# Optimization experiments

Measured on AMD Instinct MI355X. Metric: run time of the kernel, lower is better.

The kernel has to match this reference:

```python
import jax, jax.numpy as jnp
import numpy as np

B, S, E, H = 1, 2048, 1024, 16
D = E // H          # head_dim = 64
SM_SCALE = 0.5      # module default, not 1/sqrt(D)


def setup_inputs() -> dict:
    key = jax.random.key(0)
    ks = jax.random.split(key, 9)
    std = 0.02
    return {
        "x":  jax.random.normal(ks[0], (B, S, E), dtype=jnp.float32),
        "Wq": jax.random.normal(ks[1], (E, E), dtype=jnp.float32) * std,
        "bq": jnp.zeros((E,), dtype=jnp.float32),
        "Wk": jax.random.normal(ks[2], (E, E), dtype=jnp.float32) * std,
        "bk": jnp.zeros((E,), dtype=jnp.float32),
        "Wv": jax.random.normal(ks[3], (E, E), dtype=jnp.float32) * std,
        "bv": jnp.zeros((E,), dtype=jnp.float32),
        "Wo": jax.random.normal(ks[4], (E, E), dtype=jnp.float32) * std,
        "bo": jnp.zeros((E,), dtype=jnp.float32),
    }


def _split_heads(t):
    # [B,S,E] -> [B,H,S,D]
    b, s, _ = t.shape
    return jnp.transpose(t.reshape(b, s, H, D), (0, 2, 1, 3))


def reference(x, Wq, bq, Wk, bk, Wv, bv, Wo, bo):
    # Projections in fp32, then cast to bf16 (matches module's .astype(bf16))
    q = _split_heads((x @ Wq + bq).astype(jnp.bfloat16))
    k = _split_heads((x @ Wk + bk).astype(jnp.bfloat16))
    v = _split_heads((x @ Wv + bv).astype(jnp.bfloat16))

    # Blockwise loop in the original is mathematically full causal attention
    scores = jnp.einsum("bhqd,bhkd->bhqk", q, k) * SM_SCALE  # [B,H,S,S] bf16
    causal = jnp.tril(jnp.ones((S, S), dtype=bool))
    scores = jnp.where(causal[None, None, :, :], scores, -jnp.inf)
    probs = jax.nn.softmax(scores, axis=-1)
    out = jnp.einsum("bhqk,bhkd->bhqd", probs, v)            # [B,H,S,D]

    out = jnp.transpose(out, (0, 2, 1, 3)).reshape(B, S, E)
    # dropout off (is_training=False / rate=0); final projection in fp32
    return out.astype(jnp.float32) @ Wo + bo
```

## Files before the change

kernel.cpp:

```cpp
#include <hip/hip_runtime.h>
#include <hip/hip_bf16.h>

#define S_LEN 2048
#define E_DIM 1024
#define NH    16
#define HD    64
#define SM_SCALE 0.5f

typedef short bf16x8_t __attribute__((ext_vector_type(8)));
typedef float f32x4_t  __attribute__((ext_vector_type(4)));
typedef __bf16 bf16x4_t __attribute__((ext_vector_type(4)));

static __device__ __forceinline__ unsigned short f2bf_bits(float f) {
    return __builtin_bit_cast(unsigned short, (__bf16)f);
}

#define GLD16(gp, lp) __builtin_amdgcn_global_load_lds(                       \
    (const __attribute__((address_space(1))) void*)(gp),                      \
    (__attribute__((address_space(3))) void*)(lp), 16, 0, 0)

__global__ void k_prep(const float* __restrict__ x,
                       const float* __restrict__ Wq, const float* __restrict__ Wk,
                       const float* __restrict__ Wv, const float* __restrict__ Wo,
                       __bf16* __restrict__ xb, __bf16* __restrict__ wt) {
    const int z = blockIdx.z;
    if (z < 4) {
        __shared__ float tile[32][33];
        const float* W = z == 0 ? Wq : z == 1 ? Wk : z == 2 ? Wv : Wo;
        __bf16* o = wt + (size_t)z * E_DIM * E_DIM;
        const int tx = threadIdx.x, ty = threadIdx.y;
        const int bx = blockIdx.x * 32, by = blockIdx.y * 32;
#pragma unroll
        for (int j = 0; j < 32; j += 8)
            tile[ty + j][tx] = W[(size_t)(by + ty + j) * E_DIM + bx + tx];
        __syncthreads();
#pragma unroll
        for (int j = 0; j < 32; j += 8)
            o[(size_t)(bx + ty + j) * E_DIM + by + tx] = (__bf16)tile[tx][ty + j];
    } else {
        const int bid = (z - 4) * 1024 + blockIdx.y * 32 + blockIdx.x;
        const int tid = threadIdx.y * 32 + threadIdx.x;
        const int i = bid * 256 + tid;
        const float4 v = ((const float4*)x)[i];
        bf16x4_t o4;
        o4.x = (__bf16)v.x; o4.y = (__bf16)v.y; o4.z = (__bf16)v.z; o4.w = (__bf16)v.w;
        ((bf16x4_t*)xb)[i] = o4;
    }
}

__global__ __launch_bounds__(256) void k_gemm_qkv(
    const __bf16* __restrict__ xb, const __bf16* __restrict__ wt,
    const float* __restrict__ bq, const float* __restrict__ bk, const float* __restrict__ bv,
    __bf16* __restrict__ qkv) {
    __shared__ __align__(16) unsigned short As[64 * 32];
    __shared__ __align__(16) unsigned short Bs[128 * 32];

    const int z = blockIdx.z;
    const __bf16* Bt = wt + (size_t)z * E_DIM * E_DIM;
    const float* bias = z == 0 ? bq : z == 1 ? bk : bv;
    __bf16* out = qkv + (size_t)z * NH * S_LEN * HD;

    const int tid = threadIdx.x, w = tid >> 6, l = tid & 63;
    const int lm = l & 15, q4 = l >> 4;
    const int bm = blockIdx.y, bn = blockIdx.x;
    const int wm = w >> 1, wn = w & 1;

    const int sm = (w << 4) + (l >> 2);
    const int skk = (l & 3) << 3;
    const __bf16* Ag = xb + (size_t)(bm * 64 + sm) * E_DIM + skk;
    const __bf16* Bg = Bt + (size_t)(bn * 128 + sm) * E_DIM + skk;
    unsigned short* AsW = As + (w << 9);
    unsigned short* BsW = Bs + (w << 9);

    f32x4_t acc[2][4];
#pragma unroll
    for (int i = 0; i < 2; i++)
#pragma unroll
        for (int j = 0; j < 4; j++) { acc[i][j].x = 0.f; acc[i][j].y = 0.f; acc[i][j].z = 0.f; acc[i][j].w = 0.f; }

    for (int k0 = 0; k0 < E_DIM; k0 += 32) {
        __syncthreads();
        GLD16(Ag + k0, AsW);
        GLD16(Bg + k0, BsW);
        GLD16(Bg + (size_t)64 * E_DIM + k0, BsW + 2048);
        __syncthreads();

        bf16x8_t af[2], bfr[4];
#pragma unroll
        for (int mt = 0; mt < 2; mt++)
            af[mt] = *(const bf16x8_t*)&As[(wm * 32 + mt * 16 + lm) * 32 + q4 * 8];
#pragma unroll
        for (int nt = 0; nt < 4; nt++)
            bfr[nt] = *(const bf16x8_t*)&Bs[(wn * 64 + nt * 16 + lm) * 32 + q4 * 8];
#pragma unroll
        for (int mt = 0; mt < 2; mt++)
#pragma unroll
            for (int nt = 0; nt < 4; nt++)
                acc[mt][nt] = __builtin_amdgcn_mfma_f32_16x16x32_bf16(af[mt], bfr[nt], acc[mt][nt], 0, 0, 0);
    }

#pragma unroll
    for (int nt = 0; nt < 4; nt++) {
        const int n = bn * 128 + wn * 64 + nt * 16 + lm;
        const float bval = bias[n];
        const int h = n >> 6, d = n & 63;
        if (z == 2) {
            const int t4 = d >> 4, flm = d & 15;
#pragma unroll
            for (int mt = 0; mt < 2; mt++) {
                const int q4p = (mt * 2 + (q4 >> 1)) & 3;
                const int j0 = (q4 & 1) * 4;
                __bf16* ob = out + ((((size_t)h * 32 + bm) * 4 + t4) * 2 + wm) * 512
                                 + (q4p * 16 + flm) * 8 + j0;
                union { unsigned short s[4]; uint2 u; } pk;
#pragma unroll
                for (int i = 0; i < 4; i++) pk.s[i] = f2bf_bits(acc[mt][nt][i] + bval);
                *(uint2*)ob = pk.u;
            }
        } else {
            const float scale = (z == 0) ? SM_SCALE : 1.0f;
            const int c = d >> 5, q4p = (d >> 3) & 3, j = d & 7;
#pragma unroll
            for (int mt = 0; mt < 2; mt++) {
                const int s0 = bm * 64 + wm * 32 + mt * 16;
                const int kt6 = s0 >> 6, t4 = (s0 >> 4) & 3;
                __bf16* ob = out + ((((size_t)h * 32 + kt6) * 4 + t4) * 2 + c) * 512
                                 + (q4p * 16 + q4 * 4) * 8 + j;
#pragma unroll
                for (int i = 0; i < 4; i++)
                    ob[i * 8] = (__bf16)((acc[mt][nt][i] + bval) * scale);
            }
        }
    }
}

__global__ __launch_bounds__(256, 2) void k_attn(
    const __bf16* __restrict__ Qf, const __bf16* __restrict__ Kf, const __bf16* __restrict__ Vf,
    __bf16* __restrict__ attn) {
    __shared__ __align__(16) unsigned short KVs[2][2][4096];
    __shared__ __align__(16) unsigned short Pl[4][16 * 72];

    const int b = blockIdx.x;
    int qt, h;
    if (b < 256) { qt = 16 + (b >> 4); h = b & 15; }
    else         { qt = 15 - ((b - 256) >> 4); h = (b - 256) & 15; }

    const int tid = threadIdx.x, w = tid >> 6, l = tid & 63;
    const int lm = l & 15, q4 = l >> 4;

    const __bf16* Qb = Qf + ((size_t)h * 32 + qt) * 4096;
    const __bf16* Kb = Kf + (size_t)h * 32 * 4096;
    const __bf16* Vb = Vf + (size_t)h * 32 * 4096;

    bf16x8_t qf[2];
#pragma unroll
    for (int c = 0; c < 2; c++)
        qf[c] = *(const bf16x8_t*)(Qb + ((w * 2 + c) << 9) + l * 8);

    float lacc = 0.f;
    f32x4_t oacc[4];
#pragma unroll
    for (int t = 0; t < 4; t++) { oacc[t].x = 0.f; oacc[t].y = 0.f; oacc[t].z = 0.f; oacc[t].w = 0.f; }

    unsigned short* Pw = Pl[w];

    {
        const __bf16* Kg = Kb;
        const __bf16* Vg = Vb;
        GLD16(Kg + (w << 9) + l * 8,      &KVs[0][0][(w << 9) + l * 8]);
        GLD16(Kg + ((w + 4) << 9) + l * 8, &KVs[0][0][((w + 4) << 9) + l * 8]);
        GLD16(Vg + (w << 9) + l * 8,      &KVs[0][1][(w << 9) + l * 8]);
        GLD16(Vg + ((w + 4) << 9) + l * 8, &KVs[0][1][((w + 4) << 9) + l * 8]);
    }
    __syncthreads();

    for (int s = 0; s <= qt; s++) {
        const int bb = s & 1;
        if (s < qt) {
            const __bf16* Kg = Kb + (size_t)(s + 1) * 4096;
            const __bf16* Vg = Vb + (size_t)(s + 1) * 4096;
            GLD16(Kg + (w << 9) + l * 8,      &KVs[bb ^ 1][0][(w << 9) + l * 8]);
            GLD16(Kg + ((w + 4) << 9) + l * 8, &KVs[bb ^ 1][0][((w + 4) << 9) + l * 8]);
            GLD16(Vg + (w << 9) + l * 8,      &KVs[bb ^ 1][1][(w << 9) + l * 8]);
            GLD16(Vg + ((w + 4) << 9) + l * 8, &KVs[bb ^ 1][1][((w + 4) << 9) + l * 8]);
        }

        f32x4_t st[4];
#pragma unroll
        for (int t = 0; t < 4; t++) { st[t].x = 0.f; st[t].y = 0.f; st[t].z = 0.f; st[t].w = 0.f; }
#pragma unroll
        for (int t = 0; t < 4; t++) {
            bf16x8_t kf0 = *(const bf16x8_t*)&KVs[bb][0][((t * 2 + 0) << 9) + l * 8];
            bf16x8_t kf1 = *(const bf16x8_t*)&KVs[bb][0][((t * 2 + 1) << 9) + l * 8];
            st[t] = __builtin_amdgcn_mfma_f32_16x16x32_bf16(kf0, qf[0], st[t], 0, 0, 0);
            st[t] = __builtin_amdgcn_mfma_f32_16x16x32_bf16(kf1, qf[1], st[t], 0, 0, 0);
        }
        if (s == qt) {
            const int rowl = w * 16 + lm;
#pragma unroll
            for (int t = 0; t < 4; t++)
#pragma unroll
                for (int i = 0; i < 4; i++) {
                    const int keyl = t * 16 + q4 * 4 + i;
                    st[t][i] = (keyl > rowl) ? 0.f : __expf(st[t][i]);
                }
        } else {
#pragma unroll
            for (int t = 0; t < 4; t++)
#pragma unroll
                for (int i = 0; i < 4; i++) st[t][i] = __expf(st[t][i]);
        }
#pragma unroll
        for (int t = 0; t < 4; t++)
            lacc += (st[t][0] + st[t][1]) + (st[t][2] + st[t][3]);
#pragma unroll
        for (int t = 0; t < 4; t++) {
            union { unsigned short s4[4]; uint2 u; } pk;
#pragma unroll
            for (int i = 0; i < 4; i++) pk.s4[i] = f2bf_bits(st[t][i]);
            *(uint2*)&Pw[lm * 72 + t * 16 + q4 * 4] = pk.u;
        }
#pragma unroll
        for (int c = 0; c < 2; c++) {
            bf16x8_t pf = *(const bf16x8_t*)&Pw[lm * 72 + c * 32 + q4 * 8];
#pragma unroll
            for (int t = 0; t < 4; t++) {
                bf16x8_t vf = *(const bf16x8_t*)&KVs[bb][1][((t * 2 + c) << 9) + l * 8];
                oacc[t] = __builtin_amdgcn_mfma_f32_16x16x32_bf16(vf, pf, oacc[t], 0, 0, 0);
            }
        }
        __syncthreads();
    }

    lacc += __shfl_xor(lacc, 16, 64);
    lacc += __shfl_xor(lacc, 32, 64);
    const float rl = 1.f / lacc;
    const int row = qt * 64 + w * 16 + lm;
#pragma unroll
    for (int t = 0; t < 4; t++) {
        union { unsigned short s4[4]; uint2 u; } pk;
#pragma unroll
        for (int i = 0; i < 4; i++) pk.s4[i] = f2bf_bits(oacc[t][i] * rl);
        *(uint2*)(attn + (size_t)row * E_DIM + h * HD + t * 16 + q4 * 4) = pk.u;
    }
}

__global__ __launch_bounds__(256) void k_gemm_out(
    const __bf16* __restrict__ A, const __bf16* __restrict__ Bt,
    const float* __restrict__ bias, float* __restrict__ out) {
    __shared__ __align__(16) unsigned short As[64 * 32];
    __shared__ __align__(16) unsigned short Bs[128 * 32];

    const int tid = threadIdx.x, w = tid >> 6, l = tid & 63;
    const int lm = l & 15, q4 = l >> 4;
    const int bm = blockIdx.y, bn = blockIdx.x;
    const int wm = w >> 1, wn = w & 1;

    const int sm = (w << 4) + (l >> 2);
    const int skk = (l & 3) << 3;
    const __bf16* Ag = A + (size_t)(bm * 64 + sm) * E_DIM + skk;
    const __bf16* Bg = Bt + (size_t)(bn * 128 + sm) * E_DIM + skk;
    unsigned short* AsW = As + (w << 9);
    unsigned short* BsW = Bs + (w << 9);

    f32x4_t acc[2][4];
#pragma unroll
    for (int i = 0; i < 2; i++)
#pragma unroll
        for (int j = 0; j < 4; j++) { acc[i][j].x = 0.f; acc[i][j].y = 0.f; acc[i][j].z = 0.f; acc[i][j].w = 0.f; }

    for (int k0 = 0; k0 < E_DIM; k0 += 32) {
        __syncthreads();
        GLD16(Ag + k0, AsW);
        GLD16(Bg + k0, BsW);
        GLD16(Bg + (size_t)64 * E_DIM + k0, BsW + 2048);
        __syncthreads();

        bf16x8_t af[2], bfr[4];
#pragma unroll
        for (int mt = 0; mt < 2; mt++)
            af[mt] = *(const bf16x8_t*)&As[(wm * 32 + mt * 16 + lm) * 32 + q4 * 8];
#pragma unroll
        for (int nt = 0; nt < 4; nt++)
            bfr[nt] = *(const bf16x8_t*)&Bs[(wn * 64 + nt * 16 + lm) * 32 + q4 * 8];
#pragma unroll
        for (int mt = 0; mt < 2; mt++)
#pragma unroll
            for (int nt = 0; nt < 4; nt++)
                acc[mt][nt] = __builtin_amdgcn_mfma_f32_16x16x32_bf16(af[mt], bfr[nt], acc[mt][nt], 0, 0, 0);
    }

#pragma unroll
    for (int nt = 0; nt < 4; nt++) {
        const int n = bn * 128 + wn * 64 + nt * 16 + lm;
        const float bval = bias[n];
#pragma unroll
        for (int mt = 0; mt < 2; mt++) {
            const int r0 = bm * 64 + wm * 32 + mt * 16 + q4 * 4;
#pragma unroll
            for (int i = 0; i < 4; i++)
                out[(size_t)(r0 + i) * E_DIM + n] = acc[mt][nt][i] + bval;
        }
    }
}

extern "C" void kernel_launch(void* const* d_in, const int* in_sizes, int n_in,
                              void* d_out, int out_size, void* d_ws, size_t ws_size,
                              hipStream_t stream) {
    const float* x  = (const float*)d_in[0];
    const float* Wq = (const float*)d_in[1];
    const float* bq = (const float*)d_in[2];
    const float* Wk = (const float*)d_in[3];
    const float* bk = (const float*)d_in[4];
    const float* Wv = (const float*)d_in[5];
    const float* bv = (const float*)d_in[6];
    const float* Wo = (const float*)d_in[7];
    const float* bo = (const float*)d_in[8];
    float* out = (float*)d_out;

    char* ws = (char*)d_ws;
    __bf16* xb   = (__bf16*)(ws);
    __bf16* wt   = (__bf16*)(ws + ((size_t)4  << 20));
    __bf16* qkv  = (__bf16*)(ws + ((size_t)12 << 20));
    __bf16* attn = (__bf16*)(ws + ((size_t)24 << 20));

    k_prep<<<dim3(32, 32, 6), dim3(32, 8), 0, stream>>>(x, Wq, Wk, Wv, Wo, xb, wt);
    k_gemm_qkv<<<dim3(E_DIM / 128, S_LEN / 64, 3), 256, 0, stream>>>(xb, wt, bq, bk, bv, qkv);
    k_attn<<<dim3(512), 256, 0, stream>>>(
        qkv, qkv + (size_t)NH * S_LEN * HD, qkv + (size_t)2 * NH * S_LEN * HD, attn);
    k_gemm_out<<<dim3(E_DIM / 128, S_LEN / 64), 256, 0, stream>>>(
        attn, wt + (size_t)3 * E_DIM * E_DIM, bo, out);
}
```

Measured before the change: 155.8 us.

## Enlarge QKV GEMM tile to 128x128 and double-buffer output projection GEMM

The QKV projection GEMM now computes 128x128 tiles per block, so each wave handles a 64x64 sub-tile with 16 MFMAs per k-step. This improves operand reuse from LDS and halves the grid, and the epilogue's head-tiled output index math is rewritten to match. The output projection GEMM gets double-buffered LDS with the next k-slice prefetched during MFMA work, which removes one barrier per iteration. The trade-offs are higher register and LDS use, and fewer blocks for the QKV GEMM (384), which may lower occupancy.

```diff
diff --git a/kernel.cpp b/kernel.cpp
--- a/kernel.cpp
+++ b/kernel.cpp
@@ -52,7 +52,7 @@
     const __bf16* __restrict__ xb, const __bf16* __restrict__ wt,
     const float* __restrict__ bq, const float* __restrict__ bk, const float* __restrict__ bv,
     __bf16* __restrict__ qkv) {
-    __shared__ __align__(16) unsigned short As[64 * 32];
+    __shared__ __align__(16) unsigned short As[128 * 32];
     __shared__ __align__(16) unsigned short Bs[128 * 32];
 
     const int z = blockIdx.z;
@@ -67,33 +67,34 @@
 
     const int sm = (w << 4) + (l >> 2);
     const int skk = (l & 3) << 3;
-    const __bf16* Ag = xb + (size_t)(bm * 64 + sm) * E_DIM + skk;
+    const __bf16* Ag = xb + (size_t)(bm * 128 + sm) * E_DIM + skk;
     const __bf16* Bg = Bt + (size_t)(bn * 128 + sm) * E_DIM + skk;
     unsigned short* AsW = As + (w << 9);
     unsigned short* BsW = Bs + (w << 9);
 
-    f32x4_t acc[2][4];
-#pragma unroll
-    for (int i = 0; i < 2; i++)
+    f32x4_t acc[4][4];
+#pragma unroll
+    for (int i = 0; i < 4; i++)
 #pragma unroll
         for (int j = 0; j < 4; j++) { acc[i][j].x = 0.f; acc[i][j].y = 0.f; acc[i][j].z = 0.f; acc[i][j].w = 0.f; }
 
     for (int k0 = 0; k0 < E_DIM; k0 += 32) {
         __syncthreads();
         GLD16(Ag + k0, AsW);
+        GLD16(Ag + (size_t)64 * E_DIM + k0, AsW + 2048);
         GLD16(Bg + k0, BsW);
         GLD16(Bg + (size_t)64 * E_DIM + k0, BsW + 2048);
         __syncthreads();
 
-        bf16x8_t af[2], bfr[4];
-#pragma unroll
-        for (int mt = 0; mt < 2; mt++)
-            af[mt] = *(const bf16x8_t*)&As[(wm * 32 + mt * 16 + lm) * 32 + q4 * 8];
+        bf16x8_t af[4], bfr[4];
+#pragma unroll
+        for (int mt = 0; mt < 4; mt++)
+            af[mt] = *(const bf16x8_t*)&As[(wm * 64 + mt * 16 + lm) * 32 + q4 * 8];
 #pragma unroll
         for (int nt = 0; nt < 4; nt++)
             bfr[nt] = *(const bf16x8_t*)&Bs[(wn * 64 + nt * 16 + lm) * 32 + q4 * 8];
 #pragma unroll
-        for (int mt = 0; mt < 2; mt++)
+        for (int mt = 0; mt < 4; mt++)
 #pragma unroll
             for (int nt = 0; nt < 4; nt++)
                 acc[mt][nt] = __builtin_amdgcn_mfma_f32_16x16x32_bf16(af[mt], bfr[nt], acc[mt][nt], 0, 0, 0);
@@ -104,13 +105,14 @@
         const int n = bn * 128 + wn * 64 + nt * 16 + lm;
         const float bval = bias[n];
         const int h = n >> 6, d = n & 63;
+        const int tile0 = bm * 2 + wm;
         if (z == 2) {
             const int t4 = d >> 4, flm = d & 15;
 #pragma unroll
-            for (int mt = 0; mt < 2; mt++) {
+            for (int mt = 0; mt < 4; mt++) {
                 const int q4p = (mt * 2 + (q4 >> 1)) & 3;
                 const int j0 = (q4 & 1) * 4;
-                __bf16* ob = out + ((((size_t)h * 32 + bm) * 4 + t4) * 2 + wm) * 512
+                __bf16* ob = out + ((((size_t)h * 32 + tile0) * 4 + t4) * 2 + (mt >> 1)) * 512
                                  + (q4p * 16 + flm) * 8 + j0;
                 union { unsigned short s[4]; uint2 u; } pk;
 #pragma unroll
@@ -121,10 +123,8 @@
             const float scale = (z == 0) ? SM_SCALE : 1.0f;
             const int c = d >> 5, q4p = (d >> 3) & 3, j = d & 7;
 #pragma unroll
-            for (int mt = 0; mt < 2; mt++) {
-                const int s0 = bm * 64 + wm * 32 + mt * 16;
-                const int kt6 = s0 >> 6, t4 = (s0 >> 4) & 3;
-                __bf16* ob = out + ((((size_t)h * 32 + kt6) * 4 + t4) * 2 + c) * 512
+            for (int mt = 0; mt < 4; mt++) {
+                __bf16* ob = out + ((((size_t)h * 32 + tile0) * 4 + mt) * 2 + c) * 512
                                  + (q4p * 16 + q4 * 4) * 8 + j;
 #pragma unroll
                 for (int i = 0; i < 4; i++)
@@ -165,12 +165,10 @@
     unsigned short* Pw = Pl[w];
 
     {
-        const __bf16* Kg = Kb;
-        const __bf16* Vg = Vb;
-        GLD16(Kg + (w << 9) + l * 8,      &KVs[0][0][(w << 9) + l * 8]);
-        GLD16(Kg + ((w + 4) << 9) + l * 8, &KVs[0][0][((w + 4) << 9) + l * 8]);
-        GLD16(Vg + (w << 9) + l * 8,      &KVs[0][1][(w << 9) + l * 8]);
-        GLD16(Vg + ((w + 4) << 9) + l * 8, &KVs[0][1][((w + 4) << 9) + l * 8]);
+        GLD16(Kb + (w << 9) + l * 8,       &KVs[0][0][(w << 9) + l * 8]);
+        GLD16(Kb + ((w + 4) << 9) + l * 8, &KVs[0][0][((w + 4) << 9) + l * 8]);
+        GLD16(Vb + (w << 9) + l * 8,       &KVs[0][1][(w << 9) + l * 8]);
+        GLD16(Vb + ((w + 4) << 9) + l * 8, &KVs[0][1][((w + 4) << 9) + l * 8]);
     }
     __syncthreads();
 
@@ -179,9 +177,9 @@
         if (s < qt) {
             const __bf16* Kg = Kb + (size_t)(s + 1) * 4096;
             const __bf16* Vg = Vb + (size_t)(s + 1) * 4096;
-            GLD16(Kg + (w << 9) + l * 8,      &KVs[bb ^ 1][0][(w << 9) + l * 8]);
+            GLD16(Kg + (w << 9) + l * 8,       &KVs[bb ^ 1][0][(w << 9) + l * 8]);
             GLD16(Kg + ((w + 4) << 9) + l * 8, &KVs[bb ^ 1][0][((w + 4) << 9) + l * 8]);
-            GLD16(Vg + (w << 9) + l * 8,      &KVs[bb ^ 1][1][(w << 9) + l * 8]);
+            GLD16(Vg + (w << 9) + l * 8,       &KVs[bb ^ 1][1][(w << 9) + l * 8]);
             GLD16(Vg + ((w + 4) << 9) + l * 8, &KVs[bb ^ 1][1][((w + 4) << 9) + l * 8]);
         }
 
@@ -248,8 +246,8 @@
 __global__ __launch_bounds__(256) void k_gemm_out(
     const __bf16* __restrict__ A, const __bf16* __restrict__ Bt,
     const float* __restrict__ bias, float* __restrict__ out) {
-    __shared__ __align__(16) unsigned short As[64 * 32];
-    __shared__ __align__(16) unsigned short Bs[128 * 32];
+    __shared__ __align__(16) unsigned short As[2][64 * 32];
+    __shared__ __align__(16) unsigned short Bs[2][128 * 32];
 
     const int tid = threadIdx.x, w = tid >> 6, l = tid & 63;
     const int lm = l & 15, q4 = l >> 4;
@@ -260,8 +258,7 @@
     const int skk = (l & 3) << 3;
     const __bf16* Ag = A + (size_t)(bm * 64 + sm) * E_DIM + skk;
     const __bf16* Bg = Bt + (size_t)(bn * 128 + sm) * E_DIM + skk;
-    unsigned short* AsW = As + (w << 9);
-    unsigned short* BsW = Bs + (w << 9);
+    const int woff = w << 9;
 
     f32x4_t acc[2][4];
 #pragma unroll
@@ -269,25 +266,33 @@
 #pragma unroll
         for (int j = 0; j < 4; j++) { acc[i][j].x = 0.f; acc[i][j].y = 0.f; acc[i][j].z = 0.f; acc[i][j].w = 0.f; }
 
-    for (int k0 = 0; k0 < E_DIM; k0 += 32) {
-        __syncthreads();
-        GLD16(Ag + k0, AsW);
-        GLD16(Bg + k0, BsW);
-        GLD16(Bg + (size_t)64 * E_DIM + k0, BsW + 2048);
-        __syncthreads();
+    GLD16(Ag, &As[0][woff]);
+    GLD16(Bg, &Bs[0][woff]);
+    GLD16(Bg + (size_t)64 * E_DIM, &Bs[0][woff + 2048]);
+    __syncthreads();
+
+    for (int s = 0; s < 32; s++) {
+        const int bb = s & 1;
+        if (s < 31) {
+            const int k0 = (s + 1) * 32;
+            GLD16(Ag + k0, &As[bb ^ 1][woff]);
+            GLD16(Bg + k0, &Bs[bb ^ 1][woff]);
+            GLD16(Bg + (size_t)64 * E_DIM + k0, &Bs[bb ^ 1][woff + 2048]);
+        }
 
         bf16x8_t af[2], bfr[4];
 #pragma unroll
         for (int mt = 0; mt < 2; mt++)
-            af[mt] = *(const bf16x8_t*)&As[(wm * 32 + mt * 16 + lm) * 32 + q4 * 8];
+            af[mt] = *(const bf16x8_t*)&As[bb][(wm * 32 + mt * 16 + lm) * 32 + q4 * 8];
 #pragma unroll
         for (int nt = 0; nt < 4; nt++)
-            bfr[nt] = *(const bf16x8_t*)&Bs[(wn * 64 + nt * 16 + lm) * 32 + q4 * 8];
+            bfr[nt] = *(const bf16x8_t*)&Bs[bb][(wn * 64 + nt * 16 + lm) * 32 + q4 * 8];
 #pragma unroll
         for (int mt = 0; mt < 2; mt++)
 #pragma unroll
             for (int nt = 0; nt < 4; nt++)
                 acc[mt][nt] = __builtin_amdgcn_mfma_f32_16x16x32_bf16(af[mt], bfr[nt], acc[mt][nt], 0, 0, 0);
+        __syncthreads();
     }
 
 #pragma unroll
@@ -325,7 +330,7 @@
     __bf16* attn = (__bf16*)(ws + ((size_t)24 << 20));
 
     k_prep<<<dim3(32, 32, 6), dim3(32, 8), 0, stream>>>(x, Wq, Wk, Wv, Wo, xb, wt);
-    k_gemm_qkv<<<dim3(E_DIM / 128, S_LEN / 64, 3), 256, 0, stream>>>(xb, wt, bq, bk, bv, qkv);
+    k_gemm_qkv<<<dim3(E_DIM / 128, S_LEN / 128, 3), 256, 0, stream>>>(xb, wt, bq, bk, bv, qkv);
     k_attn<<<dim3(512), 256, 0, stream>>>(
         qkv, qkv + (size_t)NH * S_LEN * HD, qkv + (size_t)2 * NH * S_LEN * HD, attn);
     k_gemm_out<<<dim3(E_DIM / 128, S_LEN / 64), 256, 0, stream>>>(
```

New measurement: 157.4 us. Within noise of the previous version (+1.0%).
